# Kernel tuning notes

Measured on AMD Instinct MI355X. Metric: run time of the kernel, lower is better.

The kernel has to match this reference:

```python
import jax, jax.numpy as jnp
import numpy as np


def position_encoding(feature_size, d_model):
    pos = jnp.arange(feature_size, dtype=jnp.float32)[:, None]
    _2i = jnp.arange(0, d_model, 2, dtype=jnp.float32)
    ang = pos / jnp.power(10000.0, _2i / d_model)  # [F, D/2]
    pe = jnp.zeros((feature_size, d_model), dtype=jnp.float32)
    pe = pe.at[:, 0::2].set(jnp.sin(ang))
    pe = pe.at[:, 1::2].set(jnp.cos(ang))
    return pe


def setup_inputs() -> dict:
    key = jax.random.key(0)
    ks = jax.random.split(key, 11)
    B, F, D, T, V = 32, 512, 256, 32, 128
    sc = 0.02
    return {
        "f": jax.random.normal(ks[0], (B, F, D), dtype=jnp.float32),
        "decoder_input_ids": jax.random.randint(ks[1], (B, T), 0, V),
        "emb": sc * jax.random.normal(ks[2], (V, D), dtype=jnp.float32),
        "w_e": sc * jax.random.normal(ks[3], (D, D), dtype=jnp.float32),
        "w_h": sc * jax.random.normal(ks[4], (D, D), dtype=jnp.float32),
        "w_f": sc * jax.random.normal(ks[5], (D, D), dtype=jnp.float32),
        "w_q": sc * jax.random.normal(ks[6], (D, D), dtype=jnp.float32),
        "w_s": sc * jax.random.normal(ks[7], (D, D), dtype=jnp.float32),
        "w_g": sc * jax.random.normal(ks[8], (D, 2 * D), dtype=jnp.float32),
        "w_ih": sc * jax.random.normal(ks[9], (4 * D, 2 * D), dtype=jnp.float32),
        "w_hh": sc * jax.random.normal(ks[10], (4 * D, D), dtype=jnp.float32),
    }


def reference(f, decoder_input_ids, emb, w_e, w_h, w_f, w_q, w_s, w_g, w_ih, w_hh):
    B, F, D = f.shape
    q = position_encoding(F, D)                      # [F, D]
    dec = emb[decoder_input_ids]                     # [B, T, D]
    # loop-invariant attention terms, hoisted: w_f(f) + w_q(q)
    base = jnp.einsum('bfd,od->bfo', f, w_f) + (q @ w_q.T)[None]  # [B, F, D]
    fq = f + q[None]                                 # [B, F, D]

    def step(carry, x_t):
        h, cell, s, cp = carry
        # LSTMCell (bias=False), torch gate order i, f, g, o
        xin = jnp.concatenate([x_t, cp], axis=-1)    # [B, 2D]
        gates = xin @ w_ih.T + h @ w_hh.T            # [B, 4D]
        gi, gf, gg, go = jnp.split(gates, 4, axis=-1)
        cell = jax.nn.sigmoid(gf) * cell + jax.nn.sigmoid(gi) * jnp.tanh(gg)
        h = jax.nn.sigmoid(go) * jnp.tanh(cell)
        # Bahdanau-style energy; softmax over feature (last) dim per source
        t_in = jnp.tanh((h @ w_h.T)[:, None] + base + jnp.einsum('bfd,od->bfo', s, w_s))
        e = jnp.einsum('bfd,od->bfo', t_in, w_e)     # [B, F, D]
        alpha = jax.nn.softmax(e, axis=-1)
        s = s + alpha
        c = (alpha * f).sum(1)                       # [B, D]
        cp = (alpha * fq).sum(1)                     # [B, D]
        pred = jnp.concatenate([c, h], axis=-1) @ w_g.T  # [B, D]
        return (h, cell, s, cp), pred

    z = jnp.zeros((B, D), dtype=f.dtype)
    carry0 = (z, z, jnp.zeros_like(f), z)
    _, preds = jax.lax.scan(step, carry0, jnp.swapaxes(dec, 0, 1))  # [T, B, D]
    return jnp.swapaxes(preds, 0, 1)                 # [B, T, D]
```

## Files before the change

### kernel.cpp

```cpp
#include <hip/hip_runtime.h>
#include <math.h>

#define NB 32
#define NF 512
#define ND 256
#define NT 32
#define RPB 32
#define NTILE (NF / RPB)
#define NBLK (NB * NTILE)
#define XS 260

typedef __attribute__((ext_vector_type(8))) short bf16x8;
typedef __attribute__((ext_vector_type(4))) short bf16x4;
typedef __attribute__((ext_vector_type(4))) float f32x4;

__device__ __forceinline__ float sigmoidf_(float x) { return 1.0f / (1.0f + __expf(-x)); }

__device__ __forceinline__ short f2bf(float x) {
    union { float f; unsigned u; } v; v.f = x;
    unsigned r = (v.u + 0x7FFF + ((v.u >> 16) & 1)) >> 16;
    return (short)r;
}
__device__ __forceinline__ float bf2f(short s) {
    union { unsigned u; float f; } v;
    v.u = ((unsigned)(unsigned short)s) << 16;
    return v.f;
}

#define AGENT __HIP_MEMORY_SCOPE_AGENT
__device__ __forceinline__ float AL(const float* p) {
    return __hip_atomic_load(p, __ATOMIC_RELAXED, AGENT);
}
__device__ __forceinline__ void AS(float* p, float v) {
    __hip_atomic_store(p, v, __ATOMIC_RELAXED, AGENT);
}
__device__ __forceinline__ int APOLL(int* p) {
    return __hip_atomic_fetch_add(p, 0, __ATOMIC_RELAXED, AGENT);
}
__device__ __forceinline__ void SIGNAL(int* p, int tid, int coop) {
    asm volatile("s_waitcnt vmcnt(0)" ::: "memory");
    __syncthreads();
    if (coop && tid == 0) __hip_atomic_fetch_add(p, 1, __ATOMIC_RELAXED, AGENT);
}
__device__ __forceinline__ void WAITGE(int* p, int tgt, int tid) {
    if (tid == 0) {
        while (APOLL(p) < tgt) __builtin_amdgcn_s_sleep(2);
    }
    __syncthreads();
}

__global__ void pe_kernel(float* __restrict__ q) {
    int p = blockIdx.x;
    int d = threadIdx.x;
    float i2 = (float)((d >> 1) << 1);
    float rate = expf(-9.210340371976184f * (i2 / (float)ND));
    float ang = (float)p * rate;
    q[p * ND + d] = (d & 1) ? cosf(ang) : sinf(ang);
}

__global__ void wcvt_kernel(const float* __restrict__ w, short* __restrict__ wb, int n) {
    int i = blockIdx.x * 256 + threadIdx.x;
    if (i < n) wb[i] = f2bf(w[i]);
}

__global__ void wprep_kernel(const float* __restrict__ w_ih, const float* __restrict__ w_hh,
                             const float* __restrict__ w_h, const float* __restrict__ w_g,
                             float* __restrict__ wcat, float* __restrict__ w_hT,
                             float* __restrict__ w_gT) {
    int j = blockIdx.x;
    int o = threadIdx.x;
    wcat[(size_t)j * 768 + o]       = w_ih[(size_t)j * 512 + o];
    wcat[(size_t)j * 768 + 256 + o] = w_ih[(size_t)j * 512 + 256 + o];
    wcat[(size_t)j * 768 + 512 + o] = w_hh[(size_t)j * 256 + o];
    if (j < ND)  w_hT[(size_t)j * ND + o] = w_h[(size_t)o * ND + j];
    if (j < 512) w_gT[(size_t)j * ND + o] = w_g[(size_t)o * 512 + j];
}

__global__ void qwq_kernel(const float* __restrict__ q, const float* __restrict__ w_q,
                           float* __restrict__ qwq) {
    int p = blockIdx.x;
    int o = threadIdx.x;
    __shared__ float qs[ND];
    qs[o] = q[(size_t)p * ND + o];
    __syncthreads();
    const float4* wr = (const float4*)(w_q + (size_t)o * ND);
    float acc = 0.f;
    for (int k4 = 0; k4 < ND / 4; ++k4) {
        float4 w = wr[k4];
        int k = 4 * k4;
        acc += qs[k] * w.x + qs[k + 1] * w.y + qs[k + 2] * w.z + qs[k + 3] * w.w;
    }
    qwq[(size_t)p * ND + o] = acc;
}

__global__ void base_kernel(const float* __restrict__ fin, const float* __restrict__ w_f,
                            const float* __restrict__ qwq, float* __restrict__ bsum) {
    int b = blockIdx.x / NTILE;
    int f0 = (blockIdx.x % NTILE) * RPB;
    int o = threadIdx.x;
    __shared__ float fs[RPB][ND];
    #pragma unroll
    for (int r = 0; r < RPB; ++r)
        fs[r][o] = fin[((size_t)(b * NF + f0 + r)) * ND + o];
    __syncthreads();
    float acc[RPB];
    #pragma unroll
    for (int r = 0; r < RPB; ++r) acc[r] = 0.f;
    const float4* wr = (const float4*)(w_f + (size_t)o * ND);
    for (int k4 = 0; k4 < ND / 4; ++k4) {
        float4 w = wr[k4];
        int k = 4 * k4;
        #pragma unroll
        for (int r = 0; r < RPB; ++r)
            acc[r] += fs[r][k] * w.x + fs[r][k + 1] * w.y + fs[r][k + 2] * w.z + fs[r][k + 3] * w.w;
    }
    #pragma unroll
    for (int r = 0; r < RPB; ++r)
        bsum[((size_t)(b * NF + f0 + r)) * ND + o] = acc[r] + qwq[(size_t)(f0 + r) * ND + o];
}

__global__ void __launch_bounds__(256, 2) dec_persist(
        int coop, int t0, int smask,
        const short* __restrict__ fin_bf, const int* __restrict__ ids,
        const float* __restrict__ emb, const short* __restrict__ q_bf,
        float* __restrict__ bsum,
        const float* __restrict__ wcat, const float* __restrict__ w_hT,
        const float* __restrict__ w_gT,
        const short* __restrict__ w_e_bf, const short* __restrict__ w_s_bf,
        float* __restrict__ h, float* __restrict__ cell,
        float* __restrict__ gatesT,
        float* __restrict__ cpart, float* __restrict__ cppart,
        int* __restrict__ acount, int* __restrict__ gcount, int* __restrict__ hflag,
        float* __restrict__ out) {
    int bid = blockIdx.x;
    int tid = threadIdx.x;
    int l = tid & 63;
    int wv = tid >> 6;
    int c15 = l & 15;
    int g = l >> 4;
    int c = l;
    int b = bid >> 4;
    int tile = bid & 15;
    int f0 = tile * RPB;
    int o0 = wv * 64;

    __shared__ __align__(16) short tin_bf[RPB * ND];
    __shared__ float xfer[RPB * XS];
    __shared__ float cred[2][1024];
    __shared__ float sred[RPB][5];
    char* tb = (char*)tin_bf;
    float* zl = xfer;
    float* zp = xfer;
    float* hn = xfer;
    float* hwhl = xfer + 256;

    const size_t CP = (size_t)NTILE * NB * ND;

    float4 bsv4[8];
    if (coop) {
        #pragma unroll
        for (int i = 0; i < 8; ++i) {
            int r = wv + 4 * i;
            bsv4[i] = *(const float4*)(bsum + ((size_t)(b * NF + f0 + r)) * ND + 4 * c);
        }
    }

    int tbeg = coop ? 0 : t0;
    int tend = coop ? NT : t0;

    for (int t = tbeg; t <= tend; ++t) {
        int prd = (t > 0) ? ((t - 1) & 1) : 0;

        if ((smask & 1) && t < NT) {
            if (coop) {
                if (tid == 0) {
                    while (APOLL(&acount[b]) < 16 * t) __builtin_amdgcn_s_sleep(2);
                    while (APOLL(&hflag[b]) < t) __builtin_amdgcn_s_sleep(2);
                }
                __syncthreads();
            }
            float xv = emb[(size_t)ids[b * NT + t] * ND + tid];
            float cpsum = 0.f;
            if (t > 0) {
                #pragma unroll
                for (int tl = 0; tl < NTILE; ++tl)
                    cpsum += AL(&cppart[prd * CP + ((size_t)tl * NB + b) * ND + tid]);
            }
            zl[tid] = xv;
            zl[256 + tid] = cpsum;
            zl[512 + tid] = AL(&h[(size_t)(t & 1) * NB * ND + b * ND + tid]);
            __syncthreads();
            int j0 = tile * 64 + wv * 16;
            for (int jj = 0; jj < 16; ++jj) {
                int j = j0 + jj;
                const float* wr = wcat + (size_t)j * 768;
                float s = 0.f;
                #pragma unroll
                for (int i = 0; i < 12; ++i)
                    s += wr[l + i * 64] * zl[l + i * 64];
                #pragma unroll
                for (int off = 1; off <= 32; off <<= 1)
                    s += __shfl_xor(s, off);
                if (l == 0) AS(&gatesT[(size_t)b * 1024 + j], s);
            }
            SIGNAL(&gcount[b], tid, coop);
        }

        if ((smask & 2) && t < NT && tile == 0) {
            if (coop) WAITGE(&gcount[b], 16 * (t + 1), tid);
            float gi = AL(&gatesT[(size_t)b * 1024 + tid]);
            float gf = AL(&gatesT[(size_t)b * 1024 + 256 + tid]);
            float gg = AL(&gatesT[(size_t)b * 1024 + 512 + tid]);
            float go = AL(&gatesT[(size_t)b * 1024 + 768 + tid]);
            float cold = cell[(size_t)b * ND + tid];
            float cnew = sigmoidf_(gf) * cold + sigmoidf_(gi) * tanhf(gg);
            float hval = sigmoidf_(go) * tanhf(cnew);
            cell[(size_t)b * ND + tid] = cnew;
            AS(&h[(size_t)((t + 1) & 1) * NB * ND + b * ND + tid], hval);
            SIGNAL(&hflag[b], tid, coop);
        }

        if ((smask & 2) && t > 0 && tile == 1) {
            if (coop && t == NT) {
                if (tid == 0) {
                    while (APOLL(&acount[b]) < 16 * t) __builtin_amdgcn_s_sleep(2);
                    while (APOLL(&hflag[b]) < t) __builtin_amdgcn_s_sleep(2);
                }
                __syncthreads();
            }
            float csum = 0.f;
            #pragma unroll
            for (int tl = 0; tl < NTILE; ++tl)
                csum += AL(&cpart[prd * CP + ((size_t)tl * NB + b) * ND + tid]);
            zp[tid] = csum;
            zp[256 + tid] = AL(&h[(size_t)(t & 1) * NB * ND + b * ND + tid]);
            __syncthreads();
            float p = 0.f;
            #pragma unroll 8
            for (int k = 0; k < 512; ++k)
                p += zp[k] * w_gT[(size_t)k * ND + tid];
            out[((size_t)b * NT + (t - 1)) * ND + tid] = p;
            __syncthreads();
        }

        if (t >= NT) continue;

        if (smask & 4) {
            if (coop) WAITGE(&hflag[b], t + 1, tid);
            hn[tid] = AL(&h[(size_t)((t + 1) & 1) * NB * ND + b * ND + tid]);
            __syncthreads();
            {
                float a = 0.f;
                #pragma unroll 8
                for (int k = 0; k < ND; ++k)
                    a += hn[k] * w_hT[(size_t)k * ND + tid];
                hwhl[tid] = a;
            }
            __syncthreads();

            {
                float4 hwh4 = *(const float4*)&hwhl[4 * c];
                #pragma unroll
                for (int i = 0; i < 8; ++i) {
                    int r = wv + 4 * i;
                    if (!coop)
                        bsv4[i] = *(const float4*)(bsum + ((size_t)(b * NF + f0 + r)) * ND + 4 * c);
                    bf16x4 tv;
                    tv.x = f2bf(tanhf(hwh4.x + bsv4[i].x));
                    tv.y = f2bf(tanhf(hwh4.y + bsv4[i].y));
                    tv.z = f2bf(tanhf(hwh4.z + bsv4[i].z));
                    tv.w = f2bf(tanhf(hwh4.w + bsv4[i].w));
                    *(bf16x4*)(tb + ((r * 512 + 8 * c) ^ ((r & 7) << 4))) = tv;
                }
            }
            __syncthreads();

            f32x4 acc[2][4];
            #pragma unroll
            for (int mt = 0; mt < 2; ++mt)
                #pragma unroll
                for (int nt = 0; nt < 4; ++nt)
                    acc[mt][nt] = (f32x4)0.f;
            #pragma unroll
            for (int ks = 0; ks < 8; ++ks) {
                int kb = ks * 32 + g * 8;
                bf16x8 afr[2];
                #pragma unroll
                for (int mt = 0; mt < 2; ++mt) {
                    int row = mt * 16 + c15;
                    afr[mt] = *(const bf16x8*)(tb + ((row * 512 + kb * 2) ^ ((row & 7) << 4)));
                }
                #pragma unroll
                for (int nt = 0; nt < 4; ++nt) {
                    int o = o0 + nt * 16 + c15;
                    bf16x8 bfr = *(const bf16x8*)(w_e_bf + (size_t)o * ND + kb);
                    #pragma unroll
                    for (int mt = 0; mt < 2; ++mt)
                        acc[mt][nt] = __builtin_amdgcn_mfma_f32_16x16x32_bf16(afr[mt], bfr, acc[mt][nt], 0, 0, 0);
                }
            }

            {
                float ps[2][4];
                #pragma unroll
                for (int mt = 0; mt < 2; ++mt)
                    #pragma unroll
                    for (int reg = 0; reg < 4; ++reg) ps[mt][reg] = 0.f;
                #pragma unroll
                for (int mt = 0; mt < 2; ++mt)
                    #pragma unroll
                    for (int nt = 0; nt < 4; ++nt)
                        #pragma unroll
                        for (int reg = 0; reg < 4; ++reg) {
                            float a = __expf(acc[mt][nt][reg]);
                            acc[mt][nt][reg] = a;
                            ps[mt][reg] += a;
                        }
                #pragma unroll
                for (int off = 1; off <= 8; off <<= 1)
                    #pragma unroll
                    for (int mt = 0; mt < 2; ++mt)
                        #pragma unroll
                        for (int reg = 0; reg < 4; ++reg)
                            ps[mt][reg] += __shfl_xor(ps[mt][reg], off);
                if (c15 == 0) {
                    #pragma unroll
                    for (int mt = 0; mt < 2; ++mt)
                        #pragma unroll
                        for (int reg = 0; reg < 4; ++reg)
                            sred[mt * 16 + g * 4 + reg][wv] = ps[mt][reg];
                }
                __syncthreads();
                #pragma unroll
                for (int mt = 0; mt < 2; ++mt)
                    #pragma unroll
                    for (int reg = 0; reg < 4; ++reg) {
                        int r = mt * 16 + g * 4 + reg;
                        float inv = 1.0f / (sred[r][0] + sred[r][1] + sred[r][2] + sred[r][3]);
                        #pragma unroll
                        for (int nt = 0; nt < 4; ++nt)
                            acc[mt][nt][reg] *= inv;
                    }
            }

            #pragma unroll
            for (int mt = 0; mt < 2; ++mt)
                #pragma unroll
                for (int reg = 0; reg < 4; ++reg) {
                    int r = mt * 16 + g * 4 + reg;
                    #pragma unroll
                    for (int nt = 0; nt < 4; ++nt)
                        xfer[r * XS + o0 + nt * 16 + c15] = acc[mt][nt][reg];
                }
            __syncthreads();

            {
                float4 pc4 = {0.f, 0.f, 0.f, 0.f}, pcp4 = {0.f, 0.f, 0.f, 0.f};
                #pragma unroll
                for (int i = 0; i < 8; ++i) {
                    int r = wv + 4 * i;
                    float4 a4 = *(const float4*)&xfer[r * XS + 4 * c];
                    bf16x4 f4b = *(const bf16x4*)(fin_bf + ((size_t)(b * NF + f0 + r)) * ND + 4 * c);
                    bf16x4 q4b = *(const bf16x4*)(q_bf + ((size_t)(f0 + r)) * ND + 4 * c);
                    float fx = bf2f(f4b.x), fy = bf2f(f4b.y), fz = bf2f(f4b.z), fw = bf2f(f4b.w);
                    float qx = bf2f(q4b.x), qy = bf2f(q4b.y), qz = bf2f(q4b.z), qw = bf2f(q4b.w);
                    pc4.x += a4.x * fx;  pcp4.x += a4.x * (fx + qx);
                    pc4.y += a4.y * fy;  pcp4.y += a4.y * (fy + qy);
                    pc4.z += a4.z * fz;  pcp4.z += a4.z * (fz + qz);
                    pc4.w += a4.w * fw;  pcp4.w += a4.w * (fw + qw);
                    bf16x4 av;
                    av.x = f2bf(a4.x); av.y = f2bf(a4.y); av.z = f2bf(a4.z); av.w = f2bf(a4.w);
                    *(bf16x4*)(tb + ((r * 512 + 8 * c) ^ ((r & 7) << 4))) = av;
                }
                *(float4*)&cred[0][wv * 256 + 4 * c] = pc4;
                *(float4*)&cred[1][wv * 256 + 4 * c] = pcp4;
            }
            __syncthreads();

            {
                float pc  = cred[0][tid] + cred[0][256 + tid] + cred[0][512 + tid] + cred[0][768 + tid];
                float pcp = cred[1][tid] + cred[1][256 + tid] + cred[1][512 + tid] + cred[1][768 + tid];
                AS(&cpart [(size_t)(t & 1) * CP + ((size_t)tile * NB + b) * ND + tid], pc);
                AS(&cppart[(size_t)(t & 1) * CP + ((size_t)tile * NB + b) * ND + tid], pcp);
            }

            {
                f32x4 acc2[2][4];
                #pragma unroll
                for (int mt = 0; mt < 2; ++mt)
                    #pragma unroll
                    for (int nt = 0; nt < 4; ++nt)
                        acc2[mt][nt] = (f32x4)0.f;
                #pragma unroll
                for (int ks = 0; ks < 8; ++ks) {
                    int kb = ks * 32 + g * 8;
                    bf16x8 afr[2];
                    #pragma unroll
                    for (int mt = 0; mt < 2; ++mt) {
                        int row = mt * 16 + c15;
                        afr[mt] = *(const bf16x8*)(tb + ((row * 512 + kb * 2) ^ ((row & 7) << 4)));
                    }
                    #pragma unroll
                    for (int nt = 0; nt < 4; ++nt) {
                        int o = o0 + nt * 16 + c15;
                        bf16x8 bfr = *(const bf16x8*)(w_s_bf + (size_t)o * ND + kb);
                        #pragma unroll
                        for (int mt = 0; mt < 2; ++mt)
                            acc2[mt][nt] = __builtin_amdgcn_mfma_f32_16x16x32_bf16(afr[mt], bfr, acc2[mt][nt], 0, 0, 0);
                    }
                }
                __syncthreads();
                #pragma unroll
                for (int mt = 0; mt < 2; ++mt)
                    #pragma unroll
                    for (int reg = 0; reg < 4; ++reg) {
                        int r = mt * 16 + g * 4 + reg;
                        #pragma unroll
                        for (int nt = 0; nt < 4; ++nt)
                            xfer[r * XS + o0 + nt * 16 + c15] = acc2[mt][nt][reg];
                    }
            }
            __syncthreads();

            #pragma unroll
            for (int i = 0; i < 8; ++i) {
                int r = wv + 4 * i;
                float4 x4 = *(const float4*)&xfer[r * XS + 4 * c];
                bsv4[i].x += x4.x;
                bsv4[i].y += x4.y;
                bsv4[i].z += x4.z;
                bsv4[i].w += x4.w;
                if (!coop)
                    *(float4*)(bsum + ((size_t)(b * NF + f0 + r)) * ND + 4 * c) = bsv4[i];
            }
            SIGNAL(&acount[b], tid, coop);
        }
    }
}

extern "C" void kernel_launch(void* const* d_in, const int* in_sizes, int n_in,
                              void* d_out, int out_size, void* d_ws, size_t ws_size,
                              hipStream_t stream) {
    const float* fin  = (const float*)d_in[0];
    const int*   ids  = (const int*)  d_in[1];
    const float* emb  = (const float*)d_in[2];
    const float* w_e  = (const float*)d_in[3];
    const float* w_h  = (const float*)d_in[4];
    const float* w_f  = (const float*)d_in[5];
    const float* w_q  = (const float*)d_in[6];
    const float* w_s  = (const float*)d_in[7];
    const float* w_g  = (const float*)d_in[8];
    const float* w_ih = (const float*)d_in[9];
    const float* w_hh = (const float*)d_in[10];
    float* out = (float*)d_out;
    float* ws  = (float*)d_ws;

    size_t off = 0;
    float* q      = ws + off; off += (size_t)NF * ND;
    float* qwq    = ws + off; off += (size_t)NF * ND;
    float* bsum   = ws + off; off += (size_t)NB * NF * ND;
    float* h      = ws + off; off += (size_t)2 * NB * ND;
    float* cell   = ws + off; off += (size_t)NB * ND;
    float* gatesT = ws + off; off += (size_t)NB * 1024;
    float* cpart  = ws + off; off += (size_t)2 * NTILE * NB * ND;
    float* cppart = ws + off; off += (size_t)2 * NTILE * NB * ND;
    float* wcat   = ws + off; off += (size_t)1024 * 768;
    float* w_hT   = ws + off; off += (size_t)ND * ND;
    float* w_gT   = ws + off; off += (size_t)512 * ND;
    short* w_e_bf = (short*)(ws + off); off += (size_t)ND * ND / 2;
    short* w_s_bf = (short*)(ws + off); off += (size_t)ND * ND / 2;
    short* fin_bf = (short*)(ws + off); off += (size_t)NB * NF * ND / 2;
    short* q_bf   = (short*)(ws + off); off += (size_t)NF * ND / 2;
    int*   acount = (int*)(ws + off); off += 32;
    int*   gcount = (int*)(ws + off); off += 32;
    int*   hflag  = (int*)(ws + off); off += 32;

    hipMemsetAsync(h, 0, sizeof(float) * NB * ND, stream);
    hipMemsetAsync(cell, 0, sizeof(float) * NB * ND, stream);
    hipMemsetAsync(acount, 0, sizeof(int) * 96, stream);

    pe_kernel<<<NF, ND, 0, stream>>>(q);
    wcvt_kernel<<<ND * ND / 256, 256, 0, stream>>>(w_e, w_e_bf, ND * ND);
    wcvt_kernel<<<ND * ND / 256, 256, 0, stream>>>(w_s, w_s_bf, ND * ND);
    wcvt_kernel<<<NB * NF * ND / 256, 256, 0, stream>>>(fin, fin_bf, NB * NF * ND);
    wcvt_kernel<<<NF * ND / 256, 256, 0, stream>>>(q, q_bf, NF * ND);
    wprep_kernel<<<1024, ND, 0, stream>>>(w_ih, w_hh, w_h, w_g, wcat, w_hT, w_gT);
    qwq_kernel<<<NF, ND, 0, stream>>>(q, w_q, qwq);
    base_kernel<<<NB * NTILE, ND, 0, stream>>>(fin, w_f, qwq, bsum);

    int coop1 = 1, t00 = 0, smask7 = 7;
    void* args[] = {
        (void*)&coop1, (void*)&t00, (void*)&smask7,
        (void*)&fin_bf, (void*)&ids, (void*)&emb, (void*)&q_bf, (void*)&bsum,
        (void*)&wcat, (void*)&w_hT, (void*)&w_gT,
        (void*)&w_e_bf, (void*)&w_s_bf,
        (void*)&h, (void*)&cell, (void*)&gatesT,
        (void*)&cpart, (void*)&cppart,
        (void*)&acount, (void*)&gcount, (void*)&hflag,
        (void*)&out
    };
    hipError_t e = hipLaunchCooperativeKernel((void*)dec_persist, dim3(NBLK), dim3(ND),
                                              args, 0, stream);
    if (e != hipSuccess) {
        for (int t = 0; t <= NT; ++t) {
            if (t < NT)
                dec_persist<<<NBLK, ND, 0, stream>>>(0, t, 1, fin_bf, ids, emb, q_bf, bsum,
                        wcat, w_hT, w_gT, w_e_bf, w_s_bf, h, cell, gatesT,
                        cpart, cppart, acount, gcount, hflag, out);
            dec_persist<<<NBLK, ND, 0, stream>>>(0, t, 2, fin_bf, ids, emb, q_bf, bsum,
                    wcat, w_hT, w_gT, w_e_bf, w_s_bf, h, cell, gatesT,
                    cpart, cppart, acount, gcount, hflag, out);
            if (t < NT)
                dec_persist<<<NBLK, ND, 0, stream>>>(0, t, 4, fin_bf, ids, emb, q_bf, bsum,
                        wcat, w_hT, w_gT, w_e_bf, w_s_bf, h, cell, gatesT,
                        cpart, cppart, acount, gcount, hflag, out);
        }
    }
}
```

Baseline: 2.763 ms.

## Restructure decoder step sync: centralize cp reduction, move h·w_h into LSTM block

In the persistent decoder kernel, tile 0 of each batch now reduces the 16 cppart partials once, publishes the result to a new cpz buffer and signals a new rflag counter. The other tiles first compute the gate-matvec terms that do not depend on cp, then wait for cpz and finish the cp-dependent slice. The h·w_h matvec moves into the LSTM-update block and is published via hwhbuf, so the 16 attention tiles no longer each recompute it. Cross-block loads and stores are widened to 64-bit atomics and the spin-wait sleep is lengthened, which adds a new dependency chain and may add polling latency.

```diff
diff --git a/kernel.cpp b/kernel.cpp
--- a/kernel.cpp
+++ b/kernel.cpp
@@ -34,6 +34,16 @@
 __device__ __forceinline__ void AS(float* p, float v) {
     __hip_atomic_store(p, v, __ATOMIC_RELAXED, AGENT);
 }
+__device__ __forceinline__ float2 AL2(const float* p) {
+    unsigned long long v = __hip_atomic_load((const unsigned long long*)p, __ATOMIC_RELAXED, AGENT);
+    union { unsigned long long u; float2 f; } cv; cv.u = v;
+    return cv.f;
+}
+__device__ __forceinline__ void AS2(float* p, float x, float y) {
+    union { unsigned long long u; float2 f; } cv;
+    cv.f.x = x; cv.f.y = y;
+    __hip_atomic_store((unsigned long long*)p, cv.u, __ATOMIC_RELAXED, AGENT);
+}
 __device__ __forceinline__ int APOLL(int* p) {
     return __hip_atomic_fetch_add(p, 0, __ATOMIC_RELAXED, AGENT);
 }
@@ -44,7 +54,7 @@
 }
 __device__ __forceinline__ void WAITGE(int* p, int tgt, int tid) {
     if (tid == 0) {
-        while (APOLL(p) < tgt) __builtin_amdgcn_s_sleep(2);
+        while (APOLL(p) < tgt) __builtin_amdgcn_s_sleep(8);
     }
     __syncthreads();
 }
@@ -130,7 +140,9 @@
         float* __restrict__ h, float* __restrict__ cell,
         float* __restrict__ gatesT,
         float* __restrict__ cpart, float* __restrict__ cppart,
+        float* __restrict__ cpz, float* __restrict__ hwhbuf,
         int* __restrict__ acount, int* __restrict__ gcount, int* __restrict__ hflag,
+        int* __restrict__ rflag,
         float* __restrict__ out) {
     int bid = blockIdx.x;
     int tid = threadIdx.x;
@@ -174,34 +186,82 @@
         if ((smask & 1) && t < NT) {
             if (coop) {
                 if (tid == 0) {
-                    while (APOLL(&acount[b]) < 16 * t) __builtin_amdgcn_s_sleep(2);
-                    while (APOLL(&hflag[b]) < t) __builtin_amdgcn_s_sleep(2);
+                    while (APOLL(&acount[b]) < 16 * t) __builtin_amdgcn_s_sleep(8);
+                    while (APOLL(&hflag[b]) < t) __builtin_amdgcn_s_sleep(8);
                 }
                 __syncthreads();
             }
-            float xv = emb[(size_t)ids[b * NT + t] * ND + tid];
-            float cpsum = 0.f;
-            if (t > 0) {
-                #pragma unroll
-                for (int tl = 0; tl < NTILE; ++tl)
-                    cpsum += AL(&cppart[prd * CP + ((size_t)tl * NB + b) * ND + tid]);
-            }
-            zl[tid] = xv;
-            zl[256 + tid] = cpsum;
-            zl[512 + tid] = AL(&h[(size_t)(t & 1) * NB * ND + b * ND + tid]);
-            __syncthreads();
+            zl[tid] = emb[(size_t)ids[b * NT + t] * ND + tid];
+            if (!coop) {
+                float cpsum = 0.f;
+                if (t > 0) {
+                    #pragma unroll
+                    for (int tl = 0; tl < NTILE; ++tl)
+                        cpsum += AL(&cppart[prd * CP + ((size_t)tl * NB + b) * ND + tid]);
+                }
+                zl[256 + tid] = cpsum;
+            } else if (t == 0) {
+                zl[256 + tid] = 0.f;
+            }
+            if (tid < 128) {
+                float2 hv = AL2(&h[(size_t)(t & 1) * NB * ND + b * ND + 2 * tid]);
+                zl[512 + 2 * tid]     = hv.x;
+                zl[512 + 2 * tid + 1] = hv.y;
+            }
+            if (coop && t > 0 && tile == 0) {
+                int half = tid >> 7, cp2 = tid & 127;
+                float sx = 0.f, sy = 0.f;
+                #pragma unroll
+                for (int tl2 = 0; tl2 < 8; ++tl2) {
+                    int tl = half * 8 + tl2;
+                    float2 v = AL2(&cppart[prd * CP + ((size_t)tl * NB + b) * ND + 2 * cp2]);
+                    sx += v.x; sy += v.y;
+                }
+                cred[half][2 * cp2]     = sx;
+                cred[half][2 * cp2 + 1] = sy;
+                __syncthreads();
+                if (tid < 128) {
+                    float rx = cred[0][2 * tid] + cred[1][2 * tid];
+                    float ry = cred[0][2 * tid + 1] + cred[1][2 * tid + 1];
+                    zl[256 + 2 * tid]     = rx;
+                    zl[256 + 2 * tid + 1] = ry;
+                    AS2(&cpz[(size_t)(t & 1) * NB * ND + b * ND + 2 * tid], rx, ry);
+                }
+                SIGNAL(&rflag[b], tid, coop);
+            }
+            __syncthreads();
+
             int j0 = tile * 64 + wv * 16;
+            float s13[16];
+            #pragma unroll
             for (int jj = 0; jj < 16; ++jj) {
-                int j = j0 + jj;
-                const float* wr = wcat + (size_t)j * 768;
+                const float* wr = wcat + (size_t)(j0 + jj) * 768;
                 float s = 0.f;
                 #pragma unroll
-                for (int i = 0; i < 12; ++i)
-                    s += wr[l + i * 64] * zl[l + i * 64];
-                #pragma unroll
-                for (int off = 1; off <= 32; off <<= 1)
-                    s += __shfl_xor(s, off);
-                if (l == 0) AS(&gatesT[(size_t)b * 1024 + j], s);
+                for (int i = 0; i < 4; ++i) s += wr[l + i * 64] * zl[l + i * 64];
+                #pragma unroll
+                for (int i = 8; i < 12; ++i) s += wr[l + i * 64] * zl[l + i * 64];
+                s13[jj] = s;
+            }
+            if (coop && t > 0 && tile != 0) {
+                WAITGE(&rflag[b], t, tid);
+                if (tid < 128) {
+                    float2 v = AL2(&cpz[(size_t)(t & 1) * NB * ND + b * ND + 2 * tid]);
+                    zl[256 + 2 * tid]     = v.x;
+                    zl[256 + 2 * tid + 1] = v.y;
+                }
+                __syncthreads();
+            }
+            #pragma unroll
+            for (int jj = 0; jj < 16; ++jj) {
+                const float* wr = wcat + (size_t)(j0 + jj) * 768;
+                float s = s13[jj];
+                #pragma unroll
+                for (int i = 4; i < 8; ++i) s += wr[l + i * 64] * zl[l + i * 64];
+                #pragma unroll
+                for (int off2 = 1; off2 <= 32; off2 <<= 1)
+                    s += __shfl_xor(s, off2);
+                if (l == 0) AS(&gatesT[(size_t)b * 1024 + (j0 + jj)], s);
             }
             SIGNAL(&gcount[b], tid, coop);
         }
@@ -217,23 +277,39 @@
             float hval = sigmoidf_(go) * tanhf(cnew);
             cell[(size_t)b * ND + tid] = cnew;
             AS(&h[(size_t)((t + 1) & 1) * NB * ND + b * ND + tid], hval);
+            hn[tid] = hval;
+            __syncthreads();
+            float a = 0.f;
+            #pragma unroll 8
+            for (int k = 0; k < ND; ++k)
+                a += hn[k] * w_hT[(size_t)k * ND + tid];
+            AS(&hwhbuf[(size_t)b * ND + tid], a);
             SIGNAL(&hflag[b], tid, coop);
         }
 
         if ((smask & 2) && t > 0 && tile == 1) {
             if (coop && t == NT) {
                 if (tid == 0) {
-                    while (APOLL(&acount[b]) < 16 * t) __builtin_amdgcn_s_sleep(2);
-                    while (APOLL(&hflag[b]) < t) __builtin_amdgcn_s_sleep(2);
+                    while (APOLL(&acount[b]) < 16 * t) __builtin_amdgcn_s_sleep(8);
+                    while (APOLL(&hflag[b]) < t) __builtin_amdgcn_s_sleep(8);
                 }
                 __syncthreads();
             }
-            float csum = 0.f;
-            #pragma unroll
-            for (int tl = 0; tl < NTILE; ++tl)
-                csum += AL(&cpart[prd * CP + ((size_t)tl * NB + b) * ND + tid]);
-            zp[tid] = csum;
-            zp[256 + tid] = AL(&h[(size_t)(t & 1) * NB * ND + b * ND + tid]);
+            if (tid < 128) {
+                float sx = 0.f, sy = 0.f;
+                #pragma unroll
+                for (int tl = 0; tl < NTILE; ++tl) {
+                    float2 v = AL2(&cpart[prd * CP + ((size_t)tl * NB + b) * ND + 2 * tid]);
+                    sx += v.x; sy += v.y;
+                }
+                zp[2 * tid]     = sx;
+                zp[2 * tid + 1] = sy;
+            } else {
+                int t2 = tid - 128;
+                float2 hv = AL2(&h[(size_t)(t & 1) * NB * ND + b * ND + 2 * t2]);
+                zp[256 + 2 * t2]     = hv.x;
+                zp[256 + 2 * t2 + 1] = hv.y;
+            }
             __syncthreads();
             float p = 0.f;
             #pragma unroll 8
@@ -247,14 +323,10 @@
 
         if (smask & 4) {
             if (coop) WAITGE(&hflag[b], t + 1, tid);
-            hn[tid] = AL(&h[(size_t)((t + 1) & 1) * NB * ND + b * ND + tid]);
-            __syncthreads();
-            {
-                float a = 0.f;
-                #pragma unroll 8
-                for (int k = 0; k < ND; ++k)
-                    a += hn[k] * w_hT[(size_t)k * ND + tid];
-                hwhl[tid] = a;
+            if (tid < 128) {
+                float2 hw = AL2(&hwhbuf[(size_t)b * ND + 2 * tid]);
+                hwhl[2 * tid]     = hw.x;
+                hwhl[2 * tid + 1] = hw.y;
             }
             __syncthreads();
 
@@ -378,10 +450,16 @@
             __syncthreads();
 
             {
-                float pc  = cred[0][tid] + cred[0][256 + tid] + cred[0][512 + tid] + cred[0][768 + tid];
-                float pcp = cred[1][tid] + cred[1][256 + tid] + cred[1][512 + tid] + cred[1][768 + tid];
-                AS(&cpart [(size_t)(t & 1) * CP + ((size_t)tile * NB + b) * ND + tid], pc);
-                AS(&cppart[(size_t)(t & 1) * CP + ((size_t)tile * NB + b) * ND + tid], pcp);
+                int half = tid >> 7;
+                int cp2 = tid & 127;
+                float sx = 0.f, sy = 0.f;
+                #pragma unroll
+                for (int w = 0; w < 4; ++w) {
+                    sx += cred[half][w * 256 + 2 * cp2];
+                    sy += cred[half][w * 256 + 2 * cp2 + 1];
+                }
+                float* dst = half ? cppart : cpart;
+                AS2(&dst[(size_t)(t & 1) * CP + ((size_t)tile * NB + b) * ND + 2 * cp2], sx, sy);
             }
 
             {
@@ -464,6 +542,8 @@
     float* gatesT = ws + off; off += (size_t)NB * 1024;
     float* cpart  = ws + off; off += (size_t)2 * NTILE * NB * ND;
     float* cppart = ws + off; off += (size_t)2 * NTILE * NB * ND;
+    float* cpz    = ws + off; off += (size_t)2 * NB * ND;
+    float* hwhbuf = ws + off; off += (size_t)NB * ND;
     float* wcat   = ws + off; off += (size_t)1024 * 768;
     float* w_hT   = ws + off; off += (size_t)ND * ND;
     float* w_gT   = ws + off; off += (size_t)512 * ND;
@@ -474,10 +554,11 @@
     int*   acount = (int*)(ws + off); off += 32;
     int*   gcount = (int*)(ws + off); off += 32;
     int*   hflag  = (int*)(ws + off); off += 32;
+    int*   rflag  = (int*)(ws + off); off += 32;
 
     hipMemsetAsync(h, 0, sizeof(float) * NB * ND, stream);
     hipMemsetAsync(cell, 0, sizeof(float) * NB * ND, stream);
-    hipMemsetAsync(acount, 0, sizeof(int) * 96, stream);
+    hipMemsetAsync(acount, 0, sizeof(int) * 128, stream);
 
     pe_kernel<<<NF, ND, 0, stream>>>(q);
     wcvt_kernel<<<ND * ND / 256, 256, 0, stream>>>(w_e, w_e_bf, ND * ND);
@@ -495,8 +576,8 @@
         (void*)&wcat, (void*)&w_hT, (void*)&w_gT,
         (void*)&w_e_bf, (void*)&w_s_bf,
         (void*)&h, (void*)&cell, (void*)&gatesT,
-        (void*)&cpart, (void*)&cppart,
-        (void*)&acount, (void*)&gcount, (void*)&hflag,
+        (void*)&cpart, (void*)&cppart, (void*)&cpz, (void*)&hwhbuf,
+        (void*)&acount, (void*)&gcount, (void*)&hflag, (void*)&rflag,
         (void*)&out
     };
     hipError_t e = hipLaunchCooperativeKernel((void*)dec_persist, dim3(NBLK), dim3(ND),
@@ -506,14 +587,14 @@
             if (t < NT)
                 dec_persist<<<NBLK, ND, 0, stream>>>(0, t, 1, fin_bf, ids, emb, q_bf, bsum,
                         wcat, w_hT, w_gT, w_e_bf, w_s_bf, h, cell, gatesT,
-                        cpart, cppart, acount, gcount, hflag, out);
+                        cpart, cppart, cpz, hwhbuf, acount, gcount, hflag, rflag, out);
             dec_persist<<<NBLK, ND, 0, stream>>>(0, t, 2, fin_bf, ids, emb, q_bf, bsum,
                     wcat, w_hT, w_gT, w_e_bf, w_s_bf, h, cell, gatesT,
-                    cpart, cppart, acount, gcount, hflag, out);
+                    cpart, cppart, cpz, hwhbuf, acount, gcount, hflag, rflag, out);
             if (t < NT)
                 dec_persist<<<NBLK, ND, 0, stream>>>(0, t, 4, fin_bf, ids, emb, q_bf, bsum,
                         wcat, w_hT, w_gT, w_e_bf, w_s_bf, h, cell, gatesT,
-                        cpart, cppart, acount, gcount, hflag, out);
+                        cpart, cppart, cpz, hwhbuf, acount, gcount, hflag, rflag, out);
         }
     }
 }
```

Result: slower. 6.782 ms (+145.5%).
